# Kernel tuning notes

Hardware: AMD Instinct MI355X
Metric: run time of the kernel (lower is better)

## Reference

```python
import jax, jax.numpy as jnp
import numpy as np

IN_CH = 256


def _xavier(key, shape, gain=1.0):
    # shape = (out_ch, in_ch) for a 1x1 conv weight (flattened)
    fan_out, fan_in = shape
    limit = gain * np.sqrt(6.0 / (fan_in + fan_out))
    return jax.random.uniform(key, shape, jnp.float32, -limit, limit)


def setup_inputs() -> dict:
    key = jax.random.key(0)
    ks = jax.random.split(key, 6)
    B, C, H, W = 8, IN_CH, 64, 64
    x = jax.random.normal(ks[0], (B, C, H, W), jnp.float32)
    y = jax.random.normal(ks[1], (B, C, H, W), jnp.float32)
    Wq = _xavier(ks[2], (C // 2, C))
    Wk = _xavier(ks[3], (C // 2, C))
    Wv = _xavier(ks[4], (C, C))
    Wo = _xavier(ks[5], (C, C), gain=1e-05)
    bq = jnp.zeros((C // 2,), jnp.float32)
    bk = jnp.zeros((C // 2,), jnp.float32)
    bv = jnp.zeros((C,), jnp.float32)
    bo = jnp.zeros((C,), jnp.float32)
    return {"x": x, "y": y, "Wq": Wq, "bq": bq, "Wk": Wk, "bk": bk,
            "Wv": Wv, "bv": bv, "Wo": Wo, "bo": bo}


def reference(x, y, Wq, bq, Wk, bk, Wv, bv, Wo, bo):
    B, C, H, W = x.shape
    hw = H * W
    d = C // 2
    # 1x1 convs as channel matmuls; move to [B, HW, C] layout
    xf = x.transpose(0, 2, 3, 1).reshape(B, hw, C)  # [B, HW, C]
    yf = y.transpose(0, 2, 3, 1).reshape(B, hw, C)
    q = jnp.einsum('bnc,dc->bnd', yf, Wq) + bq      # [B, HW, C/2]
    k = jnp.einsum('bnc,dc->bnd', xf, Wk) + bk      # [B, HW, C/2]
    v = jnp.einsum('bnc,ec->bne', xf, Wv) + bv      # [B, HW, C]
    scale = jnp.asarray(d, x.dtype) ** -0.5
    w = jnp.einsum('bnd,bmd->bnm', q, k) * scale    # [B, HW, HW]
    w = jax.nn.softmax(w, axis=-1)
    h = jnp.einsum('bnm,bme->bne', w, v)            # [B, HW, C]
    h = jnp.einsum('bne,fe->bnf', h, Wo) + bo
    out = xf + h
    return out.reshape(B, H, W, C).transpose(0, 3, 1, 2)
```

## Files before the change

### kernel.cpp

```cpp
#include <hip/hip_runtime.h>
#include <hip/hip_bf16.h>
#include <stdint.h>

#define NB 8
#define CH 256
#define DQ 128
#define NE 256
#define NN 4096

using bf16x8 = __attribute__((ext_vector_type(8))) __bf16;
using bf16x4 = __attribute__((ext_vector_type(4))) __bf16;
using f32x4  = __attribute__((ext_vector_type(4))) float;

__device__ __forceinline__ void gl_lds16(const void* g, void* l){
  __builtin_amdgcn_global_load_lds(
      (const __attribute__((address_space(1))) unsigned int*)g,
      (__attribute__((address_space(3))) unsigned int*)l, 16, 0, 0);
}

__global__ __launch_bounds__(256) void wprep_k(
    const float* __restrict__ Wq, const float* __restrict__ Wk,
    const float* __restrict__ Wv, const float* __restrict__ Wo,
    __bf16* __restrict__ Wb)
{
  const int bidx = blockIdx.x;
  const float* s4;  __bf16* d;  int i = bidx * 256 + threadIdx.x;
  if (bidx < 32)       { s4 = Wq; d = Wb;          }
  else if (bidx < 64)  { s4 = Wk; d = Wb + 32768;  i -= 32 * 256; }
  else if (bidx < 128) { s4 = Wv; d = Wb + 65536;  i -= 64 * 256; }
  else                 { s4 = Wo; d = Wb + 131072; i -= 128 * 256; }
  float4 v = ((const float4*)s4)[i];
  bf16x4 o; o[0]=(__bf16)v.x; o[1]=(__bf16)v.y; o[2]=(__bf16)v.z; o[3]=(__bf16)v.w;
  *(bf16x4*)(d + i * 4) = o;
}

__global__ __launch_bounds__(256) void xyprep_k(
    const float* __restrict__ x, const float* __restrict__ y,
    __bf16* __restrict__ xt, __bf16* __restrict__ yt)
{
  const int b = blockIdx.y;
  const float* src = blockIdx.z ? y : x;
  __bf16* dst      = blockIdx.z ? yt : xt;
  const int n    = blockIdx.x * 64 + (threadIdx.x & 63);
  const int cgrp = threadIdx.x >> 6;
  const float* sb = src + (size_t)b * CH * NN + n;
  __bf16* db = dst + ((size_t)b * NN + n) * CH;
#pragma unroll
  for (int cc = 0; cc < 8; ++cc) {
    const int c0 = cgrp * 64 + cc * 8;
    bf16x8 o;
#pragma unroll
    for (int s = 0; s < 8; ++s) o[s] = (__bf16)sb[(size_t)(c0 + s) * NN];
    *(bf16x8*)(db + c0) = o;
  }
}

__global__ __launch_bounds__(256) void proj_q_k(
    const __bf16* __restrict__ yt, const __bf16* __restrict__ Wqb,
    const float* __restrict__ bq, __bf16* __restrict__ Q)
{
  const int b    = blockIdx.y;
  const int w    = threadIdx.x >> 6;
  const int lane = threadIdx.x & 63;
  const int cq   = lane & 15, g = lane >> 4;
  const int n0   = blockIdx.x * 64 + w * 16;
  const float scale = 0.08838834764831845f;

  f32x4 acc[8] = {};
  const __bf16* yb = yt + ((size_t)b * NN + n0 + cq) * CH;
#pragma unroll
  for (int kc = 0; kc < 8; ++kc) {
    const int kb = kc * 32 + g * 8;
    bf16x8 af = *(const bf16x8*)(yb + kb);
#pragma unroll
    for (int ct = 0; ct < 8; ++ct) {
      bf16x8 bfr = *(const bf16x8*)(Wqb + (ct * 16 + cq) * CH + kb);
      acc[ct] = __builtin_amdgcn_mfma_f32_16x16x32_bf16(af, bfr, acc[ct], 0, 0, 0);
    }
  }
#pragma unroll
  for (int ct = 0; ct < 8; ++ct) {
    const int col = ct * 16 + cq;
    const float bias = bq[col];
#pragma unroll
    for (int r = 0; r < 4; ++r) {
      const int n = n0 + g * 4 + r;
      Q[((size_t)b * NN + n) * DQ + col] = (__bf16)((acc[ct][r] + bias) * scale);
    }
  }
}

__global__ __launch_bounds__(256) void proj_kv_k(
    const __bf16* __restrict__ xt,
    const __bf16* __restrict__ Wkb, const float* __restrict__ bk,
    const __bf16* __restrict__ Wvb, const float* __restrict__ bv,
    __bf16* __restrict__ K, __bf16* __restrict__ Vt)
{
  const int b    = blockIdx.y;
  const int w    = threadIdx.x >> 6;
  const int lane = threadIdx.x & 63;
  const int cq   = lane & 15, g = lane >> 4;
  const int n0   = blockIdx.x * 64 + w * 16;

  f32x4 acc_k[8] = {};
  f32x4 acc_v[16] = {};
  const __bf16* xb = xt + ((size_t)b * NN + n0 + cq) * CH;
#pragma unroll
  for (int kc = 0; kc < 8; ++kc) {
    const int kb = kc * 32 + g * 8;
    bf16x8 xf = *(const bf16x8*)(xb + kb);
#pragma unroll
    for (int ct = 0; ct < 8; ++ct) {
      bf16x8 wk = *(const bf16x8*)(Wkb + (ct * 16 + cq) * CH + kb);
      acc_k[ct] = __builtin_amdgcn_mfma_f32_16x16x32_bf16(xf, wk, acc_k[ct], 0, 0, 0);
    }
#pragma unroll
    for (int et = 0; et < 16; ++et) {
      bf16x8 wv = *(const bf16x8*)(Wvb + (et * 16 + cq) * CH + kb);
      acc_v[et] = __builtin_amdgcn_mfma_f32_16x16x32_bf16(wv, xf, acc_v[et], 0, 0, 0);
    }
  }
#pragma unroll
  for (int ct = 0; ct < 8; ++ct) {
    const int col = ct * 16 + cq;
    const float bias = bk[col];
#pragma unroll
    for (int r = 0; r < 4; ++r) {
      const int n = n0 + g * 4 + r;
      K[((size_t)b * NN + n) * DQ + col] = (__bf16)(acc_k[ct][r] + bias);
    }
  }
#pragma unroll
  for (int et = 0; et < 16; ++et) {
#pragma unroll
    for (int r = 0; r < 4; ++r) {
      const int e = et * 16 + g * 4 + r;
      Vt[((size_t)b * NE + e) * NN + n0 + cq] = (__bf16)(acc_v[et][r] + bv[e]);
    }
  }
}

template<int KSPLIT>
__global__ __launch_bounds__(256, 2) void attn4_k(
    const __bf16* __restrict__ Q, const __bf16* __restrict__ K,
    const __bf16* __restrict__ Vt, __bf16* __restrict__ Hout,
    float2* __restrict__ ml)
{
  __shared__ __bf16 Kt[2][32][128];
  __shared__ __bf16 Vs[2][256][32];
  __shared__ __bf16 Pw[4][32][40];

  const int tid  = threadIdx.x;
  const int w    = tid >> 6, lane = tid & 63;
  const int cq   = lane & 15, g = lane >> 4;
  const int b    = blockIdx.y;
  const int split = (KSPLIT == 2) ? blockIdx.z : 0;
  const int n0   = blockIdx.x * 128 + w * 32;
  const int kvbase = split * (NN / KSPLIT);
  const int nsteps = (NN / KSPLIT) / 32;

  const __bf16* Kb = K  + (size_t)b * NN * DQ;
  const __bf16* Vb = Vt + (size_t)b * NE * NN;

  bf16x8 qf[2][4];
#pragma unroll
  for (int qt = 0; qt < 2; ++qt) {
    const __bf16* Qb = Q + ((size_t)b * NN + n0 + qt * 16 + cq) * DQ + g * 8;
#pragma unroll
    for (int kc = 0; kc < 4; ++kc) qf[qt][kc] = *(const bf16x8*)(Qb + kc * 32);
  }

  float m[2] = {-1e30f, -1e30f};
  float l[2] = {0.f, 0.f};
  f32x4 h[2][16] = {};

#define STAGE(dst, t_)                                                       \
  do {                                                                       \
    const int kv_ = kvbase + (t_) * 32;                                      \
    const __bf16* ks_ = Kb + (size_t)kv_ * DQ;                               \
    _Pragma("unroll")                                                        \
    for (int j = 0; j < 2; ++j) {                                            \
      const int D = j * 256 + tid;                                           \
      const int row = D >> 4, c0 = D & 15;                                   \
      gl_lds16(ks_ + (size_t)row * DQ + ((c0 ^ (row & 15)) << 3),            \
               &Kt[dst][0][0] + D * 8);                                      \
    }                                                                        \
    _Pragma("unroll")                                                        \
    for (int j = 0; j < 4; ++j) {                                            \
      const int D = j * 256 + tid;                                           \
      const int e = D >> 2, c0 = D & 3;                                      \
      gl_lds16(Vb + (size_t)e * NN + kv_ + ((c0 ^ ((e >> 1) & 3)) << 3),     \
               &Vs[dst][0][0] + D * 8);                                      \
    }                                                                        \
  } while (0)

  STAGE(0, 0);
  __syncthreads();
  int cur = 0;

  for (int t = 0; t < nsteps; ++t) {
    if (t + 1 < nsteps) STAGE(cur ^ 1, t + 1);

    f32x4 s00 = {}, s01 = {}, s10 = {}, s11 = {};
#pragma unroll
    for (int kc = 0; kc < 4; ++kc) {
      bf16x8 kf0 = *(const bf16x8*)&Kt[cur][cq][((kc * 4 + g) ^ cq) * 8];
      bf16x8 kf1 = *(const bf16x8*)&Kt[cur][16 + cq][((kc * 4 + g) ^ cq) * 8];
      s00 = __builtin_amdgcn_mfma_f32_16x16x32_bf16(kf0, qf[0][kc], s00, 0, 0, 0);
      s01 = __builtin_amdgcn_mfma_f32_16x16x32_bf16(kf1, qf[0][kc], s01, 0, 0, 0);
      s10 = __builtin_amdgcn_mfma_f32_16x16x32_bf16(kf0, qf[1][kc], s10, 0, 0, 0);
      s11 = __builtin_amdgcn_mfma_f32_16x16x32_bf16(kf1, qf[1][kc], s11, 0, 0, 0);
    }
    float mx0 = fmaxf(fmaxf(fmaxf(s00[0], s00[1]), fmaxf(s00[2], s00[3])),
                      fmaxf(fmaxf(s01[0], s01[1]), fmaxf(s01[2], s01[3])));
    float mx1 = fmaxf(fmaxf(fmaxf(s10[0], s10[1]), fmaxf(s10[2], s10[3])),
                      fmaxf(fmaxf(s11[0], s11[1]), fmaxf(s11[2], s11[3])));
    mx0 = fmaxf(mx0, __shfl_xor(mx0, 16)); mx0 = fmaxf(mx0, __shfl_xor(mx0, 32));
    mx1 = fmaxf(mx1, __shfl_xor(mx1, 16)); mx1 = fmaxf(mx1, __shfl_xor(mx1, 32));

    if (__any((mx0 > m[0] + 8.0f) | (mx1 > m[1] + 8.0f))) {
      float al[2];
      const float mn0 = fmaxf(m[0], mx0), mn1 = fmaxf(m[1], mx1);
      al[0] = __expf(m[0] - mn0); m[0] = mn0; l[0] *= al[0];
      al[1] = __expf(m[1] - mn1); m[1] = mn1; l[1] *= al[1];
#pragma unroll
      for (int qt = 0; qt < 2; ++qt) {
        float ar[4];
#pragma unroll
        for (int r = 0; r < 4; ++r) ar[r] = __shfl(al[qt], g * 4 + r);
#pragma unroll
        for (int et = 0; et < 16; ++et) {
          h[qt][et][0] *= ar[0]; h[qt][et][1] *= ar[1];
          h[qt][et][2] *= ar[2]; h[qt][et][3] *= ar[3];
        }
      }
    }
#pragma unroll
    for (int qt = 0; qt < 2; ++qt) {
      const f32x4 sa = qt ? s10 : s00;
      const f32x4 sb = qt ? s11 : s01;
      float p0[4], p1[4];
#pragma unroll
      for (int r = 0; r < 4; ++r) { p0[r] = __expf(sa[r] - m[qt]); }
#pragma unroll
      for (int r = 0; r < 4; ++r) { p1[r] = __expf(sb[r] - m[qt]); }
      float rs = (p0[0] + p0[1]) + (p0[2] + p0[3])
               + (p1[0] + p1[1]) + (p1[2] + p1[3]);
      rs += __shfl_xor(rs, 16); rs += __shfl_xor(rs, 32);
      l[qt] += rs;
      bf16x4 w0, w1;
#pragma unroll
      for (int r = 0; r < 4; ++r) { w0[r] = (__bf16)p0[r]; w1[r] = (__bf16)p1[r]; }
      *(bf16x4*)&Pw[w][qt * 16 + cq][g * 4]      = w0;
      *(bf16x4*)&Pw[w][qt * 16 + cq][16 + g * 4] = w1;
    }
    bf16x8 pa0 = *(const bf16x8*)&Pw[w][cq][g * 8];
    bf16x8 pa1 = *(const bf16x8*)&Pw[w][16 + cq][g * 8];
#pragma unroll
    for (int et = 0; et < 16; ++et) {
      bf16x8 vf = *(const bf16x8*)&Vs[cur][et * 16 + cq][(g ^ ((cq >> 1) & 3)) * 8];
      h[0][et] = __builtin_amdgcn_mfma_f32_16x16x32_bf16(pa0, vf, h[0][et], 0, 0, 0);
      h[1][et] = __builtin_amdgcn_mfma_f32_16x16x32_bf16(pa1, vf, h[1][et], 0, 0, 0);
    }
    __syncthreads();
    cur ^= 1;
  }
#undef STAGE

  if (KSPLIT == 1) {
#pragma unroll
    for (int qt = 0; qt < 2; ++qt) {
      const float inv = 1.0f / l[qt];
      float ir[4];
#pragma unroll
      for (int r = 0; r < 4; ++r) ir[r] = __shfl(inv, g * 4 + r);
#pragma unroll
      for (int et = 0; et < 16; ++et) {
#pragma unroll
        for (int r = 0; r < 4; ++r) {
          const int n = n0 + qt * 16 + g * 4 + r;
          Hout[((size_t)b * NN + n) * NE + et * 16 + cq] =
              (__bf16)(h[qt][et][r] * ir[r]);
        }
      }
    }
  } else {
#pragma unroll
    for (int qt = 0; qt < 2; ++qt) {
#pragma unroll
      for (int et = 0; et < 16; ++et) {
#pragma unroll
        for (int r = 0; r < 4; ++r) {
          const int n = n0 + qt * 16 + g * 4 + r;
          Hout[(((size_t)split * NB + b) * NN + n) * NE + et * 16 + cq] =
              (__bf16)h[qt][et][r];
        }
      }
    }
    if (g == 0) {
#pragma unroll
      for (int qt = 0; qt < 2; ++qt)
        ml[((size_t)split * NB + b) * NN + n0 + qt * 16 + cq] =
            make_float2(m[qt], l[qt]);
    }
  }
}

template<int KS>
__global__ __launch_bounds__(256) void outproj_k(
    const __bf16* __restrict__ Hp, const float2* __restrict__ ml,
    const __bf16* __restrict__ Wob, const float* __restrict__ bo,
    const float* __restrict__ x, float* __restrict__ out)
{
  const int b    = blockIdx.y;
  const int w    = threadIdx.x >> 6;
  const int lane = threadIdx.x & 63;
  const int cq   = lane & 15, g = lane >> 4;
  const int n0   = blockIdx.x * 64 + w * 16;

  const size_t row = (size_t)b * NN + n0 + cq;
  float w0 = 1.f, w1 = 0.f;
  const __bf16* Hb0 = Hp + row * NE;
  const __bf16* Hb1 = Hb0;
  if (KS == 2) {
    const float2 a = ml[row];
    const float2 c = ml[(size_t)NB * NN + row];
    const float M  = fmaxf(a.x, c.x);
    const float e0 = __expf(a.x - M), e1 = __expf(c.x - M);
    const float inv = 1.0f / (e0 * a.y + e1 * c.y);
    w0 = e0 * inv; w1 = e1 * inv;
    Hb1 = Hp + ((size_t)NB * NN + row) * NE;
  }

  f32x4 acc[16] = {};
#pragma unroll
  for (int kc = 0; kc < 8; ++kc) {
    const int kb = kc * 32 + g * 8;
    bf16x8 h0 = *(const bf16x8*)(Hb0 + kb);
    bf16x8 hf;
    if (KS == 2) {
      bf16x8 h1 = *(const bf16x8*)(Hb1 + kb);
#pragma unroll
      for (int s = 0; s < 8; ++s)
        hf[s] = (__bf16)(w0 * (float)h0[s] + w1 * (float)h1[s]);
    } else {
      hf = h0;
    }
#pragma unroll
    for (int ft = 0; ft < 16; ++ft) {
      bf16x8 wo = *(const bf16x8*)(Wob + (ft * 16 + cq) * CH + kb);
      acc[ft] = __builtin_amdgcn_mfma_f32_16x16x32_bf16(wo, hf, acc[ft], 0, 0, 0);
    }
  }
#pragma unroll
  for (int ft = 0; ft < 16; ++ft) {
#pragma unroll
    for (int r = 0; r < 4; ++r) {
      const int f = ft * 16 + g * 4 + r;
      const size_t idx = ((size_t)b * CH + f) * NN + n0 + cq;
      out[idx] = x[idx] + acc[ft][r] + bo[f];
    }
  }
}

extern "C" void kernel_launch(void* const* d_in, const int* in_sizes, int n_in,
                              void* d_out, int out_size, void* d_ws, size_t ws_size,
                              hipStream_t stream) {
  const float* x  = (const float*)d_in[0];
  const float* y  = (const float*)d_in[1];
  const float* Wq = (const float*)d_in[2];
  const float* bq = (const float*)d_in[3];
  const float* Wk = (const float*)d_in[4];
  const float* bk = (const float*)d_in[5];
  const float* Wv = (const float*)d_in[6];
  const float* bv = (const float*)d_in[7];
  const float* Wo = (const float*)d_in[8];
  const float* bo = (const float*)d_in[9];
  float* out = (float*)d_out;

  char* ws = (char*)d_ws;
  __bf16* xt = (__bf16*)(ws);
  __bf16* yt = (__bf16*)(ws + ((size_t)16 << 20));
  __bf16* Q  = (__bf16*)(ws + ((size_t)32 << 20));
  __bf16* K  = (__bf16*)(ws + ((size_t)40 << 20));
  __bf16* Vt = (__bf16*)(ws + ((size_t)48 << 20));
  __bf16* Wb = (__bf16*)(ws + ((size_t)64 << 20));
  float2* ml = (float2*)(ws + ((size_t)64 << 20) + 393216);
  __bf16* Hp = xt;
  __bf16* Wqb = Wb, *Wkb = Wb + 32768, *Wvb = Wb + 65536, *Wob = Wb + 131072;

  dim3 grid(64, 8), blk(256);
  wprep_k  <<<dim3(192), blk, 0, stream>>>(Wq, Wk, Wv, Wo, Wb);
  xyprep_k <<<dim3(64, 8, 2), blk, 0, stream>>>(x, y, xt, yt);
  proj_q_k <<<grid, blk, 0, stream>>>(yt, Wqb, bq, Q);
  proj_kv_k<<<grid, blk, 0, stream>>>(xt, Wkb, bk, Wvb, bv, K, Vt);

  const size_t need = ((size_t)64 << 20) + 393216
                    + (size_t)2 * NB * NN * sizeof(float2);
  if (ws_size >= need) {
    attn4_k<2><<<dim3(32, 8, 2), blk, 0, stream>>>(Q, K, Vt, Hp, ml);
    outproj_k<2><<<grid, blk, 0, stream>>>(Hp, ml, Wob, bo, x, out);
  } else {
    attn4_k<1><<<dim3(32, 8, 1), blk, 0, stream>>>(Q, K, Vt, Hp, nullptr);
    outproj_k<1><<<grid, blk, 0, stream>>>(Hp, nullptr, Wob, bo, x, out);
  }
}
```

Measured before the change: 359.8 us.

## Fuse input transpose/convert with Q/K/V projections via swizzled LDS staging

Replaces the separate transpose-to-bf16 kernel and the two projection kernels with one kernel. It loads 64 spatial positions of x and y, converts them to bf16 into XOR-swizzled shared memory, and then computes Q, K and V from LDS. This removes the bf16 xt/yt round trip through global memory and two launches. In exchange it uses 64KB of LDS per block, which may limit occupancy, and each block computes all three projections serially.

```diff
diff --git a/kernel.cpp b/kernel.cpp
--- a/kernel.cpp
+++ b/kernel.cpp
@@ -34,110 +34,110 @@
   *(bf16x4*)(d + i * 4) = o;
 }
 
-__global__ __launch_bounds__(256) void xyprep_k(
+__global__ __launch_bounds__(256) void projall_k(
     const float* __restrict__ x, const float* __restrict__ y,
-    __bf16* __restrict__ xt, __bf16* __restrict__ yt)
-{
-  const int b = blockIdx.y;
-  const float* src = blockIdx.z ? y : x;
-  __bf16* dst      = blockIdx.z ? yt : xt;
-  const int n    = blockIdx.x * 64 + (threadIdx.x & 63);
-  const int cgrp = threadIdx.x >> 6;
-  const float* sb = src + (size_t)b * CH * NN + n;
-  __bf16* db = dst + ((size_t)b * NN + n) * CH;
-#pragma unroll
-  for (int cc = 0; cc < 8; ++cc) {
-    const int c0 = cgrp * 64 + cc * 8;
-    bf16x8 o;
-#pragma unroll
-    for (int s = 0; s < 8; ++s) o[s] = (__bf16)sb[(size_t)(c0 + s) * NN];
-    *(bf16x8*)(db + c0) = o;
-  }
-}
-
-__global__ __launch_bounds__(256) void proj_q_k(
-    const __bf16* __restrict__ yt, const __bf16* __restrict__ Wqb,
-    const float* __restrict__ bq, __bf16* __restrict__ Q)
-{
-  const int b    = blockIdx.y;
-  const int w    = threadIdx.x >> 6;
-  const int lane = threadIdx.x & 63;
-  const int cq   = lane & 15, g = lane >> 4;
-  const int n0   = blockIdx.x * 64 + w * 16;
-  const float scale = 0.08838834764831845f;
-
-  f32x4 acc[8] = {};
-  const __bf16* yb = yt + ((size_t)b * NN + n0 + cq) * CH;
-#pragma unroll
-  for (int kc = 0; kc < 8; ++kc) {
-    const int kb = kc * 32 + g * 8;
-    bf16x8 af = *(const bf16x8*)(yb + kb);
-#pragma unroll
-    for (int ct = 0; ct < 8; ++ct) {
-      bf16x8 bfr = *(const bf16x8*)(Wqb + (ct * 16 + cq) * CH + kb);
-      acc[ct] = __builtin_amdgcn_mfma_f32_16x16x32_bf16(af, bfr, acc[ct], 0, 0, 0);
-    }
-  }
-#pragma unroll
-  for (int ct = 0; ct < 8; ++ct) {
-    const int col = ct * 16 + cq;
-    const float bias = bq[col];
-#pragma unroll
-    for (int r = 0; r < 4; ++r) {
-      const int n = n0 + g * 4 + r;
-      Q[((size_t)b * NN + n) * DQ + col] = (__bf16)((acc[ct][r] + bias) * scale);
-    }
-  }
-}
-
-__global__ __launch_bounds__(256) void proj_kv_k(
-    const __bf16* __restrict__ xt,
+    const __bf16* __restrict__ Wqb, const float* __restrict__ bq,
     const __bf16* __restrict__ Wkb, const float* __restrict__ bk,
     const __bf16* __restrict__ Wvb, const float* __restrict__ bv,
-    __bf16* __restrict__ K, __bf16* __restrict__ Vt)
+    __bf16* __restrict__ Q, __bf16* __restrict__ K, __bf16* __restrict__ Vt)
 {
-  const int b    = blockIdx.y;
-  const int w    = threadIdx.x >> 6;
-  const int lane = threadIdx.x & 63;
+  __shared__ __bf16 Xs[64 * 256];
+  __shared__ __bf16 Ys[64 * 256];
+
+  const int tid = threadIdx.x;
+  const int b   = blockIdx.y;
+  const int n0  = blockIdx.x * 64;
+
+  {
+    const int ln = tid & 63;
+    const int cg = tid >> 6;
+    const float* xb = x + (size_t)b * CH * NN + n0 + ln;
+    const float* yb = y + (size_t)b * CH * NN + n0 + ln;
+#pragma unroll
+    for (int i = 0; i < 8; ++i) {
+      const int c8 = cg + i * 4;
+      const int c0 = c8 * 8;
+      bf16x8 ox, oy;
+#pragma unroll
+      for (int s = 0; s < 8; ++s) {
+        ox[s] = (__bf16)xb[(size_t)(c0 + s) * NN];
+        oy[s] = (__bf16)yb[(size_t)(c0 + s) * NN];
+      }
+      const int ch = c8 ^ (ln & 15);
+      *(bf16x8*)&Xs[(ln * 32 + ch) * 8] = ox;
+      *(bf16x8*)&Ys[(ln * 32 + ch) * 8] = oy;
+    }
+  }
+  __syncthreads();
+
+  const int w    = tid >> 6;
+  const int lane = tid & 63;
   const int cq   = lane & 15, g = lane >> 4;
-  const int n0   = blockIdx.x * 64 + w * 16;
-
-  f32x4 acc_k[8] = {};
-  f32x4 acc_v[16] = {};
-  const __bf16* xb = xt + ((size_t)b * NN + n0 + cq) * CH;
-#pragma unroll
-  for (int kc = 0; kc < 8; ++kc) {
-    const int kb = kc * 32 + g * 8;
-    bf16x8 xf = *(const bf16x8*)(xb + kb);
+  const int nw   = n0 + w * 16;
+  const float scale = 0.08838834764831845f;
+
+#define LDA(S, kc) (*(const bf16x8*)&S[(((w * 16 + cq) * 32) + (((kc) * 4 + g) ^ cq)) * 8])
+
+  {
+    f32x4 acc[8] = {};
+#pragma unroll
+    for (int kc = 0; kc < 8; ++kc) {
+      bf16x8 af = LDA(Ys, kc);
+#pragma unroll
+      for (int ct = 0; ct < 8; ++ct) {
+        bf16x8 bfr = *(const bf16x8*)(Wqb + (ct * 16 + cq) * CH + kc * 32 + g * 8);
+        acc[ct] = __builtin_amdgcn_mfma_f32_16x16x32_bf16(af, bfr, acc[ct], 0, 0, 0);
+      }
+    }
 #pragma unroll
     for (int ct = 0; ct < 8; ++ct) {
-      bf16x8 wk = *(const bf16x8*)(Wkb + (ct * 16 + cq) * CH + kb);
-      acc_k[ct] = __builtin_amdgcn_mfma_f32_16x16x32_bf16(xf, wk, acc_k[ct], 0, 0, 0);
+      const int col = ct * 16 + cq;
+      const float bias = bq[col];
+#pragma unroll
+      for (int r = 0; r < 4; ++r) {
+        const int n = nw + g * 4 + r;
+        Q[((size_t)b * NN + n) * DQ + col] = (__bf16)((acc[ct][r] + bias) * scale);
+      }
+    }
+  }
+
+  {
+    f32x4 acc_k[8] = {};
+    f32x4 acc_v[16] = {};
+#pragma unroll
+    for (int kc = 0; kc < 8; ++kc) {
+      bf16x8 xf = LDA(Xs, kc);
+#pragma unroll
+      for (int ct = 0; ct < 8; ++ct) {
+        bf16x8 wk = *(const bf16x8*)(Wkb + (ct * 16 + cq) * CH + kc * 32 + g * 8);
+        acc_k[ct] = __builtin_amdgcn_mfma_f32_16x16x32_bf16(xf, wk, acc_k[ct], 0, 0, 0);
+      }
+#pragma unroll
+      for (int et = 0; et < 16; ++et) {
+        bf16x8 wv = *(const bf16x8*)(Wvb + (et * 16 + cq) * CH + kc * 32 + g * 8);
+        acc_v[et] = __builtin_amdgcn_mfma_f32_16x16x32_bf16(wv, xf, acc_v[et], 0, 0, 0);
+      }
+    }
+#pragma unroll
+    for (int ct = 0; ct < 8; ++ct) {
+      const int col = ct * 16 + cq;
+      const float bias = bk[col];
+#pragma unroll
+      for (int r = 0; r < 4; ++r) {
+        const int n = nw + g * 4 + r;
+        K[((size_t)b * NN + n) * DQ + col] = (__bf16)(acc_k[ct][r] + bias);
+      }
     }
 #pragma unroll
     for (int et = 0; et < 16; ++et) {
-      bf16x8 wv = *(const bf16x8*)(Wvb + (et * 16 + cq) * CH + kb);
-      acc_v[et] = __builtin_amdgcn_mfma_f32_16x16x32_bf16(wv, xf, acc_v[et], 0, 0, 0);
-    }
-  }
-#pragma unroll
-  for (int ct = 0; ct < 8; ++ct) {
-    const int col = ct * 16 + cq;
-    const float bias = bk[col];
-#pragma unroll
-    for (int r = 0; r < 4; ++r) {
-      const int n = n0 + g * 4 + r;
-      K[((size_t)b * NN + n) * DQ + col] = (__bf16)(acc_k[ct][r] + bias);
-    }
-  }
-#pragma unroll
-  for (int et = 0; et < 16; ++et) {
-#pragma unroll
-    for (int r = 0; r < 4; ++r) {
-      const int e = et * 16 + g * 4 + r;
-      Vt[((size_t)b * NE + e) * NN + n0 + cq] = (__bf16)(acc_v[et][r] + bv[e]);
-    }
-  }
+#pragma unroll
+      for (int r = 0; r < 4; ++r) {
+        const int e = et * 16 + g * 4 + r;
+        Vt[((size_t)b * NE + e) * NN + nw + cq] = (__bf16)(acc_v[et][r] + bv[e]);
+      }
+    }
+  }
+#undef LDA
 }
 
 template<int KSPLIT>
@@ -379,21 +379,17 @@
   float* out = (float*)d_out;
 
   char* ws = (char*)d_ws;
-  __bf16* xt = (__bf16*)(ws);
-  __bf16* yt = (__bf16*)(ws + ((size_t)16 << 20));
+  __bf16* Hp = (__bf16*)(ws);
   __bf16* Q  = (__bf16*)(ws + ((size_t)32 << 20));
   __bf16* K  = (__bf16*)(ws + ((size_t)40 << 20));
   __bf16* Vt = (__bf16*)(ws + ((size_t)48 << 20));
   __bf16* Wb = (__bf16*)(ws + ((size_t)64 << 20));
   float2* ml = (float2*)(ws + ((size_t)64 << 20) + 393216);
-  __bf16* Hp = xt;
   __bf16* Wqb = Wb, *Wkb = Wb + 32768, *Wvb = Wb + 65536, *Wob = Wb + 131072;
 
   dim3 grid(64, 8), blk(256);
   wprep_k  <<<dim3(192), blk, 0, stream>>>(Wq, Wk, Wv, Wo, Wb);
-  xyprep_k <<<dim3(64, 8, 2), blk, 0, stream>>>(x, y, xt, yt);
-  proj_q_k <<<grid, blk, 0, stream>>>(yt, Wqb, bq, Q);
-  proj_kv_k<<<grid, blk, 0, stream>>>(xt, Wkb, bk, Wvb, bv, K, Vt);
+  projall_k<<<grid, blk, 0, stream>>>(x, y, Wqb, bq, Wkb, bk, Wvb, bv, Q, K, Vt);
 
   const size_t need = ((size_t)64 << 20) + 393216
                     + (size_t)2 * NB * NN * sizeof(float2);
```

After: 346.1 us. 1.04x faster.
